# Kernel tuning notes

Measured on AMD Instinct MI355X. Metric: run time of the kernel, lower is better.

Reference implementation:

```python
import jax, jax.numpy as jnp
import numpy as np

B, N, NR, D = 1024, 100000, 500, 200
OC, FW = 32, 9          # out_channels, filt_w (filt_h is always 1)
L = D - FW + 1          # 192, conv output width
EPS = 1e-5


def setup_inputs() -> dict:
    key = jax.random.key(0)
    ks = jax.random.split(key, 22)
    inp = {
        "e1_idx": jax.random.randint(ks[0], (B,), 0, N),
        "r_idx": jax.random.randint(ks[1], (B,), 0, NR),
        "E": jax.random.normal(ks[2], (N, D), jnp.float32) * 0.1,
        "R": jax.random.normal(ks[3], (NR, D), jnp.float32) * 0.1,
        "W_fc": jax.random.normal(ks[4], (OC * L, D), jnp.float32) * 0.02,
        "b_fc": jnp.zeros((D,), jnp.float32),
        "W_fc1": jax.random.normal(ks[5], (D, OC * FW), jnp.float32) * 0.05,
        "b_fc1": jnp.zeros((OC * FW,), jnp.float32),
        "bn0_g": jax.random.uniform(ks[6], (1,), jnp.float32, 0.5, 1.5),
        "bn0_b": jax.random.normal(ks[7], (1,), jnp.float32) * 0.1,
        "bn0_m": jax.random.normal(ks[8], (1,), jnp.float32) * 0.1,
        "bn0_v": jax.random.uniform(ks[9], (1,), jnp.float32, 0.5, 1.5),
        "bn1_g": jax.random.uniform(ks[10], (OC,), jnp.float32, 0.5, 1.5),
        "bn1_b": jax.random.normal(ks[11], (OC,), jnp.float32) * 0.1,
        "bn1_m": jax.random.normal(ks[12], (OC,), jnp.float32) * 0.1,
        "bn1_v": jax.random.uniform(ks[13], (OC,), jnp.float32, 0.5, 1.5),
        "bn2_g": jax.random.uniform(ks[14], (D,), jnp.float32, 0.5, 1.5),
        "bn2_b": jax.random.normal(ks[15], (D,), jnp.float32) * 0.1,
        "bn2_m": jax.random.normal(ks[16], (D,), jnp.float32) * 0.1,
        "bn2_v": jax.random.uniform(ks[17], (D,), jnp.float32, 0.5, 1.5),
        "b": jnp.zeros((N,), jnp.float32),
    }
    return inp


def reference(e1_idx, r_idx, E, R, W_fc, b_fc, W_fc1, b_fc1,
              bn0_g, bn0_b, bn0_m, bn0_v,
              bn1_g, bn1_b, bn1_m, bn1_v,
              bn2_g, bn2_b, bn2_m, bn2_v, b):
    # embeddings
    e1 = E[e1_idx]                       # [B, D]  (the [B,1,1,D] image)
    r = R[r_idx]                         # [B, D]
    # bn0 over the single input channel (eval mode, running stats)
    x = (e1 - bn0_m) * (bn0_g / jnp.sqrt(bn0_v + EPS)) + bn0_b   # [B, D]
    # hypernetwork: per-sample filters
    k = (r @ W_fc1 + b_fc1).reshape(B, OC, FW)                    # [B, OC, FW]
    # per-sample grouped conv == sliding-window batched small matmul
    idx = jnp.arange(L)[:, None] + jnp.arange(FW)[None, :]        # [L, FW]
    win = x[:, idx]                                               # [B, L, FW]
    y = jnp.einsum('blw,bow->bol', win, k)                        # [B, OC, L]
    # bn1 over OC channels (eval)
    y = (y - bn1_m[:, None]) * (bn1_g / jnp.sqrt(bn1_v + EPS))[:, None] + bn1_b[:, None]
    # fc (torch Linear: x @ W.T + b, W_fc is [fc_len, D])
    h = y.reshape(B, OC * L) @ W_fc + b_fc                        # [B, D]
    # bn2 over D features (eval) + relu
    h = (h - bn2_m) * (bn2_g / jnp.sqrt(bn2_v + EPS)) + bn2_b
    h = jax.nn.relu(h)
    # score against all entities
    logits = h @ E.T + b                                          # [B, N]
    return jax.nn.sigmoid(logits)
```

## Files before the change

### kernel.cpp

```cpp
#include <hip/hip_runtime.h>

#define B_    1024
#define N_    100000
#define NP_   100096
#define NR_   500
#define D_    200
#define KP_   224
#define OC_   32
#define FW_   9
#define L_    192
#define OCL_  6144
#define KS_   16
#define KCH_  384
#define EPS_  1e-5f

typedef __attribute__((ext_vector_type(8))) short  bf16x8;
typedef __attribute__((ext_vector_type(4))) float  f32x4;

static __device__ __forceinline__ unsigned short f2bf(float x) {
    unsigned int u = __float_as_uint(x);
    unsigned int r = (u + 0x7FFFu + ((u >> 16) & 1u)) >> 16;
    return (unsigned short)r;
}

__global__ __launch_bounds__(256) void k1(
    const int* __restrict__ e1_idx, const int* __restrict__ r_idx,
    const float* __restrict__ E, const float* __restrict__ R,
    const float* __restrict__ W_fc1, const float* __restrict__ b_fc1,
    const float* __restrict__ W_fc,
    const float* __restrict__ bn0_g, const float* __restrict__ bn0_b,
    const float* __restrict__ bn0_m, const float* __restrict__ bn0_v,
    const float* __restrict__ bn1_g, const float* __restrict__ bn1_b,
    const float* __restrict__ bn1_m, const float* __restrict__ bn1_v,
    unsigned short* __restrict__ y_bf, unsigned short* __restrict__ Wt_bf,
    unsigned short* __restrict__ E_bf)
{
    const int tid = threadIdx.x;
    const int bid = blockIdx.x;

    if (bid < B_) {
        __shared__ float x_lds[D_];
        __shared__ float r_lds[D_];
        __shared__ float k_lds[OC_ * FW_];
        __shared__ float s1_lds[OC_], t1_lds[OC_];

        const int b = bid;
        const float s0 = bn0_g[0] / sqrtf(bn0_v[0] + EPS_);
        const float c0 = bn0_b[0] - bn0_m[0] * s0;

        if (tid < D_) {
            x_lds[tid] = E[(long)e1_idx[b] * D_ + tid] * s0 + c0;
            r_lds[tid] = R[(long)r_idx[b] * D_ + tid];
        } else if (tid >= 224) {
            int o = tid - 224;
            float s1 = bn1_g[o] / sqrtf(bn1_v[o] + EPS_);
            s1_lds[o] = s1;
            t1_lds[o] = bn1_b[o] - bn1_m[o] * s1;
        }
        __syncthreads();

        for (int j = tid; j < OC_ * FW_; j += 256) {
            float acc = b_fc1[j];
            #pragma unroll 4
            for (int d = 0; d < D_; ++d)
                acc += r_lds[d] * W_fc1[d * (OC_ * FW_) + j];
            k_lds[j] = acc * s1_lds[j / FW_];
        }
        __syncthreads();

        unsigned short* yrow = y_bf + (long)b * OCL_;
        for (int idx = tid; idx < OCL_; idx += 256) {
            int o = idx / L_;
            int l = idx - o * L_;
            const float* kp = &k_lds[o * FW_];
            float acc = t1_lds[o];
            #pragma unroll
            for (int w = 0; w < FW_; ++w)
                acc += x_lds[l + w] * kp[w];
            yrow[idx] = f2bf(acc);
        }
    } else if (bid < B_ + 384) {
        __shared__ float t_lds[64][65];
        const int wb = bid - B_;
        const int k0 = (wb % 96) * 64;
        const int d0 = (wb / 96) * 64;
        const int c  = tid & 63;
        const int r4 = tid >> 6;
        #pragma unroll
        for (int i = 0; i < 16; ++i) {
            int row = i * 4 + r4;
            t_lds[row][c] = (d0 + c < D_) ? W_fc[(long)(k0 + row) * D_ + d0 + c] : 0.f;
        }
        __syncthreads();
        #pragma unroll
        for (int i = 0; i < 16; ++i) {
            int drow = i * 4 + r4;
            Wt_bf[(long)(d0 + drow) * OCL_ + k0 + c] = f2bf(t_lds[c][drow]);
        }
    } else {
        long id = (long)(bid - (B_ + 384)) * 256 + tid;
        int n = (int)(id / (KP_ / 4));
        int cc = (int)(id - (long)n * (KP_ / 4));
        ushort4 o = {0, 0, 0, 0};
        if (n < N_ && cc < D_ / 4) {
            float4 v = *(const float4*)&E[(long)n * D_ + cc * 4];
            o.x = f2bf(v.x); o.y = f2bf(v.y); o.z = f2bf(v.z); o.w = f2bf(v.w);
        }
        *(ushort4*)&E_bf[(long)n * KP_ + cc * 4] = o;
    }
}

__global__ __launch_bounds__(256) void kB(
    const unsigned short* __restrict__ y_bf, const unsigned short* __restrict__ Wt_bf,
    float* __restrict__ pre)
{
    const int wave = threadIdx.x >> 6;
    const int lane = threadIdx.x & 63;
    const int quad = lane >> 4;
    const int lc   = lane & 15;

    const int m0 = blockIdx.x * 128 + wave * 32;
    const int n0 = blockIdx.y * 64;
    const int kb = blockIdx.z * KCH_;

    f32x4 acc[2][4] = {};

    const short* a0p = (const short*)y_bf + (long)(m0 + lc) * OCL_ + kb + quad * 8;
    const short* a1p = a0p + 16 * OCL_;

    #pragma unroll
    for (int k0 = 0; k0 < KCH_; k0 += 32) {
        bf16x8 a0 = *(const bf16x8*)(a0p + k0);
        bf16x8 a1 = *(const bf16x8*)(a1p + k0);
        #pragma unroll
        for (int t = 0; t < 4; ++t) {
            bf16x8 bv = *(const bf16x8*)((const short*)Wt_bf
                         + (long)(n0 + t * 16 + lc) * OCL_ + kb + k0 + quad * 8);
            acc[0][t] = __builtin_amdgcn_mfma_f32_16x16x32_bf16(a0, bv, acc[0][t], 0, 0, 0);
            acc[1][t] = __builtin_amdgcn_mfma_f32_16x16x32_bf16(a1, bv, acc[1][t], 0, 0, 0);
        }
    }

    #pragma unroll
    for (int t = 0; t < 4; ++t) {
        int d = n0 + t * 16 + lc;
        if (d < KP_) {
            #pragma unroll
            for (int mi = 0; mi < 2; ++mi)
                #pragma unroll
                for (int r = 0; r < 4; ++r) {
                    int m = m0 + mi * 16 + quad * 4 + r;
                    pre[((long)blockIdx.z * B_ + m) * KP_ + d] = acc[mi][t][r];
                }
        }
    }
}

__global__ __launch_bounds__(256) void kB2(
    const float* __restrict__ pre, const float* __restrict__ b_fc,
    const float* __restrict__ bn2_g, const float* __restrict__ bn2_b,
    const float* __restrict__ bn2_m, const float* __restrict__ bn2_v,
    unsigned short* __restrict__ h_bf)
{
    int id = blockIdx.x * 256 + threadIdx.x;
    if (id >= B_ * KP_) return;
    int b = id / KP_;
    int d = id - b * KP_;
    float h = 0.f;
    if (d < D_) {
        float s = 0.f;
        #pragma unroll
        for (int sp = 0; sp < KS_; ++sp)
            s += pre[(long)sp * B_ * KP_ + id];
        float s2 = bn2_g[d] / sqrtf(bn2_v[d] + EPS_);
        h = (s + b_fc[d] - bn2_m[d]) * s2 + bn2_b[d];
        h = fmaxf(h, 0.f);
    }
    h_bf[id] = f2bf(h);
}

__global__ __launch_bounds__(256) void kE(
    const float* __restrict__ E, unsigned short* __restrict__ E_bf)
{
    long id = (long)blockIdx.x * 256 + threadIdx.x;
    if (id >= (long)NP_ * (KP_ / 4)) return;
    int n = (int)(id / (KP_ / 4));
    int c = (int)(id - (long)n * (KP_ / 4));
    ushort4 o = {0, 0, 0, 0};
    if (n < N_ && c < D_ / 4) {
        float4 v = *(const float4*)&E[(long)n * D_ + c * 4];
        o.x = f2bf(v.x); o.y = f2bf(v.y); o.z = f2bf(v.z); o.w = f2bf(v.w);
    }
    *(ushort4*)&E_bf[(long)n * KP_ + c * 4] = o;
}

__global__ __launch_bounds__(256) void kC(
    const unsigned short* __restrict__ h_bf, const unsigned short* __restrict__ E_bf,
    const float* __restrict__ bias, float* __restrict__ out)
{
    const int wave = threadIdx.x >> 6;
    const int lane = threadIdx.x & 63;
    const int quad = lane >> 4;
    const int lc   = lane & 15;

    const int m0 = blockIdx.x * 128 + wave * 32;
    const int n0 = blockIdx.y * 64;

    f32x4 acc[2][4] = {};

    const short* hbase0 = (const short*)h_bf + (long)(m0 + lc) * KP_ + quad * 8;
    const short* hbase1 = hbase0 + 16 * KP_;

    #pragma unroll
    for (int k0 = 0; k0 < KP_; k0 += 32) {
        bf16x8 a0 = *(const bf16x8*)(hbase0 + k0);
        bf16x8 a1 = *(const bf16x8*)(hbase1 + k0);
        #pragma unroll
        for (int t = 0; t < 4; ++t) {
            int n = n0 + t * 16 + lc;
            bf16x8 b = *(const bf16x8*)((const short*)E_bf + (long)n * KP_ + k0 + quad * 8);
            acc[0][t] = __builtin_amdgcn_mfma_f32_16x16x32_bf16(a0, b, acc[0][t], 0, 0, 0);
            acc[1][t] = __builtin_amdgcn_mfma_f32_16x16x32_bf16(a1, b, acc[1][t], 0, 0, 0);
        }
    }

    #pragma unroll
    for (int t = 0; t < 4; ++t) {
        int n = n0 + t * 16 + lc;
        if (n < N_) {
            float bv = bias[n];
            #pragma unroll
            for (int mi = 0; mi < 2; ++mi) {
                #pragma unroll
                for (int r = 0; r < 4; ++r) {
                    int m = m0 + mi * 16 + quad * 4 + r;
                    float v = acc[mi][t][r] + bv;
                    out[(long)m * N_ + n] = 1.f / (1.f + __expf(-v));
                }
            }
        }
    }
}

extern "C" void kernel_launch(void* const* d_in, const int* in_sizes, int n_in,
                              void* d_out, int out_size, void* d_ws, size_t ws_size,
                              hipStream_t stream) {
    const int*   e1_idx = (const int*)d_in[0];
    const int*   r_idx  = (const int*)d_in[1];
    const float* E      = (const float*)d_in[2];
    const float* R      = (const float*)d_in[3];
    const float* W_fc   = (const float*)d_in[4];
    const float* b_fc   = (const float*)d_in[5];
    const float* W_fc1  = (const float*)d_in[6];
    const float* b_fc1  = (const float*)d_in[7];
    const float* bn0_g  = (const float*)d_in[8];
    const float* bn0_b  = (const float*)d_in[9];
    const float* bn0_m  = (const float*)d_in[10];
    const float* bn0_v  = (const float*)d_in[11];
    const float* bn1_g  = (const float*)d_in[12];
    const float* bn1_b  = (const float*)d_in[13];
    const float* bn1_m  = (const float*)d_in[14];
    const float* bn1_v  = (const float*)d_in[15];
    const float* bn2_g  = (const float*)d_in[16];
    const float* bn2_b  = (const float*)d_in[17];
    const float* bn2_m  = (const float*)d_in[18];
    const float* bn2_v  = (const float*)d_in[19];
    const float* bias   = (const float*)d_in[20];
    float* out = (float*)d_out;

    char* base = (char*)d_ws;
    unsigned short* y_bf  = (unsigned short*)(base);
    float*          pre   = (float*)(base + 12582912L);
    unsigned short* Wt_bf = (unsigned short*)(base + 27262976L);
    unsigned short* h_bf  = (unsigned short*)(base + 44843008L);
    const size_t FLAT_NEED = 90144768UL;
    const bool flat = ws_size >= FLAT_NEED;
    unsigned short* E_bf = flat ? (unsigned short*)(base + 45301760L)
                                : (unsigned short*)(base);

    const int ECONV_BLOCKS = (int)(((long)NP_ * (KP_ / 4)) / 256);
    const int k1_blocks = flat ? (B_ + 384 + ECONV_BLOCKS) : (B_ + 384);

    k1<<<k1_blocks, 256, 0, stream>>>(e1_idx, r_idx, E, R, W_fc1, b_fc1, W_fc,
                                      bn0_g, bn0_b, bn0_m, bn0_v,
                                      bn1_g, bn1_b, bn1_m, bn1_v,
                                      y_bf, Wt_bf, E_bf);
    kB<<<dim3(8, 4, KS_), 256, 0, stream>>>(y_bf, Wt_bf, pre);
    kB2<<<(B_ * KP_ + 255) / 256, 256, 0, stream>>>(pre, b_fc, bn2_g, bn2_b, bn2_m, bn2_v, h_bf);
    if (!flat)
        kE<<<ECONV_BLOCKS, 256, 0, stream>>>(E, E_bf);
    kC<<<dim3(8, NP_ / 64), 256, 0, stream>>>(h_bf, E_bf, bias, out);
}
```

Measured before the change: 741.8 us.

## Stage E tile in swizzled LDS and vectorize sigmoid output stores via LDS transpose

The scoring GEMM kernel now loads the block's 64-row E_bf tile into shared memory once, using an XOR swizzle to avoid bank conflicts, so the four waves share it instead of each fetching B fragments from global memory. The epilogue writes accumulators plus bias to shared memory and reads them back row-major, so each lane emits float4 coalesced stores of the sigmoid output. This targets the uncoalesced scalar stores of the large 1024x100000 output and the redundant E reads. In exchange it adds LDS usage (32 KB), which may lower occupancy, and two barriers.

```diff
diff --git a/kernel.cpp b/kernel.cpp
--- a/kernel.cpp
+++ b/kernel.cpp
@@ -198,13 +198,30 @@
     const unsigned short* __restrict__ h_bf, const unsigned short* __restrict__ E_bf,
     const float* __restrict__ bias, float* __restrict__ out)
 {
-    const int wave = threadIdx.x >> 6;
-    const int lane = threadIdx.x & 63;
+    __shared__ short smem[64 * 256];
+
+    const int tid  = threadIdx.x;
+    const int wave = tid >> 6;
+    const int lane = tid & 63;
     const int quad = lane >> 4;
     const int lc   = lane & 15;
 
     const int m0 = blockIdx.x * 128 + wave * 32;
     const int n0 = blockIdx.y * 64;
+
+    {
+        const short* src = (const short*)E_bf;
+        #pragma unroll
+        for (int i = 0; i < 7; ++i) {
+            int u   = tid + i * 256;
+            int row = u / 28;
+            int c16 = u - row * 28;
+            int4 v = *(const int4*)(src + (long)(n0 + row) * KP_ + c16 * 8);
+            int c = c16 ^ (row & 7);
+            *(int4*)&smem[row * 256 + c * 8] = v;
+        }
+    }
+    __syncthreads();
 
     f32x4 acc[2][4] = {};
 
@@ -215,29 +232,47 @@
     for (int k0 = 0; k0 < KP_; k0 += 32) {
         bf16x8 a0 = *(const bf16x8*)(hbase0 + k0);
         bf16x8 a1 = *(const bf16x8*)(hbase1 + k0);
+        const int cbase = (k0 >> 3) + quad;
         #pragma unroll
         for (int t = 0; t < 4; ++t) {
-            int n = n0 + t * 16 + lc;
-            bf16x8 b = *(const bf16x8*)((const short*)E_bf + (long)n * KP_ + k0 + quad * 8);
-            acc[0][t] = __builtin_amdgcn_mfma_f32_16x16x32_bf16(a0, b, acc[0][t], 0, 0, 0);
-            acc[1][t] = __builtin_amdgcn_mfma_f32_16x16x32_bf16(a1, b, acc[1][t], 0, 0, 0);
-        }
-    }
+            int row = t * 16 + lc;
+            int c   = cbase ^ (row & 7);
+            bf16x8 bv = *(const bf16x8*)&smem[row * 256 + c * 8];
+            acc[0][t] = __builtin_amdgcn_mfma_f32_16x16x32_bf16(a0, bv, acc[0][t], 0, 0, 0);
+            acc[1][t] = __builtin_amdgcn_mfma_f32_16x16x32_bf16(a1, bv, acc[1][t], 0, 0, 0);
+        }
+    }
+
+    __syncthreads();
+    float* fw = (float*)smem + wave * 2048;
 
     #pragma unroll
     for (int t = 0; t < 4; ++t) {
         int n = n0 + t * 16 + lc;
+        float bv = (n < N_) ? bias[n] : 0.f;
+        #pragma unroll
+        for (int mi = 0; mi < 2; ++mi)
+            #pragma unroll
+            for (int r = 0; r < 4; ++r) {
+                int rl = mi * 16 + quad * 4 + r;
+                fw[rl * 64 + t * 16 + lc] = acc[mi][t][r] + bv;
+            }
+    }
+
+    #pragma unroll
+    for (int j = 0; j < 8; ++j) {
+        int u  = lane + j * 64;
+        int rl = u >> 4;
+        int c4 = u & 15;
+        int n  = n0 + c4 * 4;
         if (n < N_) {
-            float bv = bias[n];
-            #pragma unroll
-            for (int mi = 0; mi < 2; ++mi) {
-                #pragma unroll
-                for (int r = 0; r < 4; ++r) {
-                    int m = m0 + mi * 16 + quad * 4 + r;
-                    float v = acc[mi][t][r] + bv;
-                    out[(long)m * N_ + n] = 1.f / (1.f + __expf(-v));
-                }
-            }
+            float4 v = *(const float4*)&fw[rl * 64 + c4 * 4];
+            float4 o;
+            o.x = 1.f / (1.f + __expf(-v.x));
+            o.y = 1.f / (1.f + __expf(-v.y));
+            o.z = 1.f / (1.f + __expf(-v.z));
+            o.w = 1.f / (1.f + __expf(-v.w));
+            *(float4*)&out[(long)(m0 + rl) * N_ + n] = o;
         }
     }
 }
```

Measured after the change: 673.7 us. 1.1x faster.
